# Optimization experiments

Hardware: AMD Instinct MI355X
Metric: run time of the kernel (lower is better)

Reference implementation:

```python
import jax, jax.numpy as jnp
import numpy as np

N_NODES = 50000
N_EDGES = 800000
IN_DIM = 128
HID = 64
NUM_GRAPHS = 64


def _gcn_conv(x, W, b, src, dst, num_nodes):
    """PyG GCNConv: out = D^-1/2 (A+I) D^-1/2 (x W) + b, messages scattered to dst."""
    h = x @ W  # [N, out]
    ones = jnp.ones((src.shape[0],), dtype=x.dtype)
    # degree at target nodes, self-loop adds 1
    deg = jax.ops.segment_sum(ones, dst, num_segments=num_nodes) + 1.0
    dinv = jax.lax.rsqrt(deg)  # [N]
    norm = dinv[src] * dinv[dst]  # [E]
    msgs = h[src] * norm[:, None]  # [E, out] gather-scale
    agg = jax.ops.segment_sum(msgs, dst, num_segments=num_nodes)  # scatter-add
    # self-loop contribution: norm_ii = dinv[i]^2
    agg = agg + h * (dinv * dinv)[:, None]
    return agg + b


def setup_inputs() -> dict:
    key = jax.random.key(0)
    k = jax.random.split(key, 10)
    x = jax.random.normal(k[0], (N_NODES, IN_DIM), dtype=jnp.float32)
    edge_index = jax.random.randint(k[1], (2, N_EDGES), 0, N_NODES, dtype=jnp.int32)
    batch = jnp.sort(jax.random.randint(k[2], (N_NODES,), 0, NUM_GRAPHS, dtype=jnp.int32))
    # Glorot-ish params
    W1 = jax.random.normal(k[3], (IN_DIM, HID), dtype=jnp.float32) / np.sqrt(IN_DIM)
    b1 = jnp.zeros((HID,), dtype=jnp.float32)
    W2 = jax.random.normal(k[4], (HID, HID), dtype=jnp.float32) / np.sqrt(HID)
    b2 = jnp.zeros((HID,), dtype=jnp.float32)
    Wlin = jax.random.normal(k[5], (HID, 1), dtype=jnp.float32) / np.sqrt(HID)
    blin = jnp.zeros((1,), dtype=jnp.float32)
    return {"x": x, "edge_index": edge_index, "batch": batch,
            "W1": W1, "b1": b1, "W2": W2, "b2": b2, "Wlin": Wlin, "blin": blin}


def reference(x, edge_index, batch, W1, b1, W2, b2, Wlin, blin):
    src, dst = edge_index[0], edge_index[1]
    h = _gcn_conv(x, W1, b1, src, dst, N_NODES)
    h = jax.nn.relu(h)  # dropout is identity in eval mode
    h = _gcn_conv(h, W2, b2, src, dst, N_NODES)
    h = jax.nn.relu(h)
    # global mean pool per graph
    sums = jax.ops.segment_sum(h, batch, num_segments=NUM_GRAPHS)  # [G, HID]
    cnts = jax.ops.segment_sum(jnp.ones((N_NODES,), h.dtype), batch, num_segments=NUM_GRAPHS)
    pooled = sums / jnp.maximum(cnts, 1.0)[:, None]
    return pooled @ Wlin + blin  # [G, 1]
```

## Files before the change

kernel.cpp:

```cpp
#include <hip/hip_runtime.h>
#include <hip/hip_fp16.h>

#define N_NODES 50000
#define N_EDGES 800000
#define IN_DIM 128
#define HID 64
#define NUM_GRAPHS 64
#define RED_BLOCKS 128
#define NB 196
#define NBLK 256

__device__ inline float4 load_h4(const __half* p) {
    const __half2* q = (const __half2*)p;
    float2 a = __half22float2(q[0]);
    float2 b = __half22float2(q[1]);
    return make_float4(a.x, a.y, b.x, b.y);
}
__device__ inline void store_h4(__half* p, float4 v) {
    __half2* q = (__half2*)p;
    q[0] = __floats2half2_rn(v.x, v.y);
    q[1] = __floats2half2_rn(v.z, v.w);
}

__global__ __launch_bounds__(256) void hist_kernel(const int* __restrict__ dst, int* __restrict__ hist_g) {
    __shared__ int h[NB];
    int tid = threadIdx.x;
    for (int i = tid; i < NB; i += 256) h[i] = 0;
    __syncthreads();
    const int NI = N_EDGES / 4;
    for (int i = blockIdx.x * 256 + tid; i < NI; i += NBLK * 256) {
        int4 d = ((const int4*)dst)[i];
        atomicAdd(&h[d.x >> 8], 1);
        atomicAdd(&h[d.y >> 8], 1);
        atomicAdd(&h[d.z >> 8], 1);
        atomicAdd(&h[d.w >> 8], 1);
    }
    __syncthreads();
    for (int i = tid; i < NB; i += 256) hist_g[i * NBLK + blockIdx.x] = h[i];
}

__global__ __launch_bounds__(1024) void scan2_kernel(const int* __restrict__ in, int* __restrict__ pos,
                                                     int* __restrict__ offs) {
    __shared__ int wsum[16];
    __shared__ int tot_s;
    int tid = threadIdx.x;
    int lane = tid & 63, wid = tid >> 6;
    int carry = 0;
    const int L = NB * NBLK;
    for (int base = 0; base < L; base += 4096) {
        int idx = base + tid * 4;
        int v0 = 0, v1 = 0, v2 = 0, v3 = 0;
        if (idx < L) { int4 v = *(const int4*)&in[idx]; v0 = v.x; v1 = v.y; v2 = v.z; v3 = v.w; }
        int s0 = v0, s1 = s0 + v1, s2 = s1 + v2, s3 = s2 + v3;
        int inc = s3;
        #pragma unroll
        for (int d = 1; d < 64; d <<= 1) { int t = __shfl_up(inc, d, 64); if (lane >= d) inc += t; }
        if (lane == 63) wsum[wid] = inc;
        __syncthreads();
        if (tid < 16) {
            int wv = wsum[tid], winc = wv;
            #pragma unroll
            for (int d = 1; d < 16; d <<= 1) { int t = __shfl_up(winc, d, 16); if (tid >= d) winc += t; }
            wsum[tid] = winc - wv;
            if (tid == 15) tot_s = winc;
        }
        __syncthreads();
        int excl = carry + wsum[wid] + inc - s3;
        if (idx < L) { int4 o; o.x = excl; o.y = excl + s0; o.z = excl + s1; o.w = excl + s2; *(int4*)&pos[idx] = o; }
        carry += tot_s;
    }
    if (tid == 0) offs[N_NODES] = N_EDGES;
}

__global__ __launch_bounds__(256) void bin_kernel(const int* __restrict__ src, const int* __restrict__ dst,
                                                  const int* __restrict__ pos, int* __restrict__ binned) {
    __shared__ int cur[NB];
    int tid = threadIdx.x;
    for (int i = tid; i < NB; i += 256) cur[i] = pos[i * NBLK + blockIdx.x];
    __syncthreads();
    const int NI = N_EDGES / 4;
    for (int i = blockIdx.x * 256 + tid; i < NI; i += NBLK * 256) {
        int4 s = ((const int4*)src)[i];
        int4 d = ((const int4*)dst)[i];
        int p0 = atomicAdd(&cur[d.x >> 8], 1); binned[p0] = (s.x & 0xFFFF) | ((d.x & 255) << 16);
        int p1 = atomicAdd(&cur[d.y >> 8], 1); binned[p1] = (s.y & 0xFFFF) | ((d.y & 255) << 16);
        int p2 = atomicAdd(&cur[d.z >> 8], 1); binned[p2] = (s.z & 0xFFFF) | ((d.z & 255) << 16);
        int p3 = atomicAdd(&cur[d.w >> 8], 1); binned[p3] = (s.w & 0xFFFF) | ((d.w & 255) << 16);
    }
}

__global__ __launch_bounds__(256) void build_kernel(const int* __restrict__ binned, const int* __restrict__ pos,
                                                    int* __restrict__ offs, float* __restrict__ dinv,
                                                    int* __restrict__ csr_src) {
    __shared__ int cnt[256];
    __shared__ int excl[256];
    __shared__ int rnk[256];
    __shared__ int wtot[4];
    int b = blockIdx.x, tid = threadIdx.x;
    int base = pos[b * NBLK];
    int end  = (b == NB - 1) ? N_EDGES : pos[(b + 1) * NBLK];
    cnt[tid] = 0; rnk[tid] = 0;
    __syncthreads();
    for (int j = base + tid; j < end; j += 256) atomicAdd(&cnt[(binned[j] >> 16) & 255], 1);
    __syncthreads();
    int v = cnt[tid];
    int lane = tid & 63, wid = tid >> 6;
    int inc = v;
    #pragma unroll
    for (int d = 1; d < 64; d <<= 1) { int t = __shfl_up(inc, d, 64); if (lane >= d) inc += t; }
    if (lane == 63) wtot[wid] = inc;
    __syncthreads();
    if (tid == 0) {
        int a = 0;
        for (int w = 0; w < 4; w++) { int t = wtot[w]; wtot[w] = a; a += t; }
    }
    __syncthreads();
    excl[tid] = wtot[wid] + inc - v;
    int node = b * 256 + tid;
    if (node < N_NODES) {
        offs[node] = base + excl[tid];
        dinv[node] = rsqrtf((float)v + 1.0f);
    }
    __syncthreads();
    for (int j = base + tid; j < end; j += 256) {
        int e = binned[j];
        int l = (e >> 16) & 255;
        int r = atomicAdd(&rnk[l], 1);
        csr_src[base + excl[l] + r] = e & 0xFFFF;
    }
}

template <int K, typename TIN>
__global__ __launch_bounds__(256) void gemm_kernel(const TIN* __restrict__ A, const float* __restrict__ W,
                                                   const float* __restrict__ dinv,
                                                   __half* __restrict__ out, int nRows) {
    constexpr int KB = 64;
    constexpr int KBP = KB + 4;
    __shared__ float xs[64 * KBP];
    __shared__ float ws[KB * 68];
    int tid = threadIdx.x;
    int node0 = blockIdx.x * 64;
    int c0 = (tid & 15) * 4, n0 = (tid >> 4) * 4;
    float acc[4][4] = {};
    for (int kb = 0; kb < K; kb += KB) {
        for (int i = tid; i < KB * 16; i += 256) {
            int k = i >> 4, c4 = (i & 15) * 4;
            *(float4*)&ws[k * 68 + c4] = *(const float4*)&W[(size_t)(kb + k) * 64 + c4];
        }
        for (int i = tid; i < 64 * (KB / 4); i += 256) {
            int n = i / (KB / 4), k4 = (i % (KB / 4)) * 4;
            int gn = node0 + n;
            float4 v;
            if (gn < nRows) {
                if constexpr (sizeof(TIN) == 4) v = *(const float4*)&A[(size_t)gn * K + kb + k4];
                else                            v = load_h4((const __half*)&A[(size_t)gn * K + kb + k4]);
            } else v = make_float4(0.f, 0.f, 0.f, 0.f);
            *(float4*)&xs[n * KBP + k4] = v;
        }
        __syncthreads();
        for (int k = 0; k < KB; k += 4) {
            float4 x0 = *(const float4*)&xs[(n0 + 0) * KBP + k];
            float4 x1 = *(const float4*)&xs[(n0 + 1) * KBP + k];
            float4 x2 = *(const float4*)&xs[(n0 + 2) * KBP + k];
            float4 x3 = *(const float4*)&xs[(n0 + 3) * KBP + k];
            #define KSTEP(KK, F) { \
                float4 wr = *(const float4*)&ws[(k + KK) * 68 + c0]; \
                acc[0][0] += x0.F * wr.x; acc[0][1] += x0.F * wr.y; acc[0][2] += x0.F * wr.z; acc[0][3] += x0.F * wr.w; \
                acc[1][0] += x1.F * wr.x; acc[1][1] += x1.F * wr.y; acc[1][2] += x1.F * wr.z; acc[1][3] += x1.F * wr.w; \
                acc[2][0] += x2.F * wr.x; acc[2][1] += x2.F * wr.y; acc[2][2] += x2.F * wr.z; acc[2][3] += x2.F * wr.w; \
                acc[3][0] += x3.F * wr.x; acc[3][1] += x3.F * wr.y; acc[3][2] += x3.F * wr.z; acc[3][3] += x3.F * wr.w; }
            KSTEP(0, x)
            KSTEP(1, y)
            KSTEP(2, z)
            KSTEP(3, w)
            #undef KSTEP
        }
        __syncthreads();
    }
    #pragma unroll
    for (int i = 0; i < 4; i++) {
        int gn = node0 + n0 + i;
        if (gn < nRows) {
            float sc = dinv[gn];
            store_h4(&out[(size_t)gn * 64 + c0],
                     make_float4(acc[i][0] * sc, acc[i][1] * sc, acc[i][2] * sc, acc[i][3] * sc));
        }
    }
}

__global__ __launch_bounds__(256) void agg_kernel(const __half* __restrict__ hd, const int* __restrict__ offs,
                                                  const int* __restrict__ csr_src,
                                                  const float* __restrict__ dinv, const float* __restrict__ bias,
                                                  __half* __restrict__ out) {
    int lane = threadIdx.x & 63;
    int node = blockIdx.x * 4 + (threadIdx.x >> 6);
    if (node >= N_NODES) return;
    int q = lane >> 4;
    int cc = (lane & 15) * 4;
    float4 acc = make_float4(0.f, 0.f, 0.f, 0.f);
    int beg = offs[node], end = offs[node + 1];
    #pragma unroll 2
    for (int j = beg + q; j < end; j += 4) {
        int s = csr_src[j];
        float4 hv = load_h4(&hd[(size_t)s * 64 + cc]);
        acc.x += hv.x; acc.y += hv.y; acc.z += hv.z; acc.w += hv.w;
    }
    #pragma unroll
    for (int m = 16; m <= 32; m <<= 1) {
        acc.x += __shfl_xor(acc.x, m, 64);
        acc.y += __shfl_xor(acc.y, m, 64);
        acc.z += __shfl_xor(acc.z, m, 64);
        acc.w += __shfl_xor(acc.w, m, 64);
    }
    if (q == 0) {
        float di = dinv[node];
        float4 hn = load_h4(&hd[(size_t)node * 64 + cc]);
        const float4 bv = *(const float4*)&bias[cc];
        float4 r;
        r.x = fmaxf(fmaf(di, acc.x + hn.x, bv.x), 0.0f);
        r.y = fmaxf(fmaf(di, acc.y + hn.y, bv.y), 0.0f);
        r.z = fmaxf(fmaf(di, acc.z + hn.z, bv.z), 0.0f);
        r.w = fmaxf(fmaf(di, acc.w + hn.w, bv.w), 0.0f);
        store_h4(&out[(size_t)node * 64 + cc], r);
    }
}

__global__ __launch_bounds__(256) void agg2dot_kernel(const __half* __restrict__ hd, const int* __restrict__ offs,
                                                      const int* __restrict__ csr_src,
                                                      const float* __restrict__ dinv, const float* __restrict__ bias,
                                                      const float* __restrict__ Wlin,
                                                      float* __restrict__ ndot) {
    int lane = threadIdx.x & 63;
    int node = blockIdx.x * 4 + (threadIdx.x >> 6);
    if (node >= N_NODES) return;
    int q = lane >> 4;
    int cc = (lane & 15) * 4;
    float4 acc = make_float4(0.f, 0.f, 0.f, 0.f);
    int beg = offs[node], end = offs[node + 1];
    #pragma unroll 2
    for (int j = beg + q; j < end; j += 4) {
        int s = csr_src[j];
        float4 hv = load_h4(&hd[(size_t)s * 64 + cc]);
        acc.x += hv.x; acc.y += hv.y; acc.z += hv.z; acc.w += hv.w;
    }
    #pragma unroll
    for (int m = 16; m <= 32; m <<= 1) {
        acc.x += __shfl_xor(acc.x, m, 64);
        acc.y += __shfl_xor(acc.y, m, 64);
        acc.z += __shfl_xor(acc.z, m, 64);
        acc.w += __shfl_xor(acc.w, m, 64);
    }
    if (q == 0) {
        float di = dinv[node];
        float4 hn = load_h4(&hd[(size_t)node * 64 + cc]);
        const float4 bv = *(const float4*)&bias[cc];
        const float4 wl = *(const float4*)&Wlin[cc];
        float rx = fmaxf(fmaf(di, acc.x + hn.x, bv.x), 0.0f);
        float ry = fmaxf(fmaf(di, acc.y + hn.y, bv.y), 0.0f);
        float rz = fmaxf(fmaf(di, acc.z + hn.z, bv.z), 0.0f);
        float rw = fmaxf(fmaf(di, acc.w + hn.w, bv.w), 0.0f);
        float d = rx * wl.x + ry * wl.y + rz * wl.z + rw * wl.w;
        #pragma unroll
        for (int m = 1; m < 16; m <<= 1) d += __shfl_xor(d, m, 64);
        if ((lane & 15) == 0) ndot[node] = d;
    }
}

__global__ __launch_bounds__(256) void reduce_kernel(const float* __restrict__ ndot, const int* __restrict__ batch,
                                                     float* __restrict__ gpart) {
    __shared__ float lsum[NUM_GRAPHS];
    __shared__ float lcnt[NUM_GRAPHS];
    int tid = threadIdx.x;
    if (tid < NUM_GRAPHS) { lsum[tid] = 0.0f; lcnt[tid] = 0.0f; }
    __syncthreads();
    for (int i = blockIdx.x * 256 + tid; i < N_NODES; i += RED_BLOCKS * 256) {
        atomicAdd(&lsum[batch[i]], ndot[i]);
        atomicAdd(&lcnt[batch[i]], 1.0f);
    }
    __syncthreads();
    if (tid < NUM_GRAPHS) {
        gpart[(size_t)blockIdx.x * (2 * NUM_GRAPHS) + tid] = lsum[tid];
        gpart[(size_t)blockIdx.x * (2 * NUM_GRAPHS) + NUM_GRAPHS + tid] = lcnt[tid];
    }
}

__global__ __launch_bounds__(1024) void final_kernel(const float* __restrict__ gpart, const float* __restrict__ blin,
                                                     float* __restrict__ out) {
    __shared__ float rs[1024];
    __shared__ float rc[1024];
    int tid = threadIdx.x;
    int g = tid & 63;
    int c = tid >> 6;
    float s = 0.0f, cn = 0.0f;
    for (int b = c; b < RED_BLOCKS; b += 16) {
        s  += gpart[(size_t)b * (2 * NUM_GRAPHS) + g];
        cn += gpart[(size_t)b * (2 * NUM_GRAPHS) + NUM_GRAPHS + g];
    }
    rs[tid] = s; rc[tid] = cn;
    __syncthreads();
    if (c == 0) {
        float ts = 0.0f, tc = 0.0f;
        #pragma unroll
        for (int k = 0; k < 16; k++) { ts += rs[k * 64 + g]; tc += rc[k * 64 + g]; }
        out[g] = ts / fmaxf(tc, 1.0f) + blin[0];
    }
}

extern "C" void kernel_launch(void* const* d_in, const int* in_sizes, int n_in,
                              void* d_out, int out_size, void* d_ws, size_t ws_size,
                              hipStream_t stream) {
    const float* x    = (const float*)d_in[0];
    const int*   ei   = (const int*)d_in[1];
    const int*   batch= (const int*)d_in[2];
    const float* W1   = (const float*)d_in[3];
    const float* b1   = (const float*)d_in[4];
    const float* W2   = (const float*)d_in[5];
    const float* b2   = (const float*)d_in[6];
    const float* Wlin = (const float*)d_in[7];
    const float* blin = (const float*)d_in[8];
    float* out = (float*)d_out;
    const int* srcA = ei;
    const int* dstA = ei + N_EDGES;

    char* p = (char*)d_ws;
    auto alloc = [&](size_t n) { char* r = p; p += (n + 255) & ~(size_t)255; return r; };
    int*    hist_g  = (int*)alloc((size_t)NB * NBLK * 4);
    int*    pos     = (int*)alloc((size_t)NB * NBLK * 4);
    int*    offs    = (int*)alloc((size_t)(N_NODES + 1) * 4);
    int*    binned  = (int*)alloc((size_t)N_EDGES * 4);
    int*    csr_src = (int*)alloc((size_t)N_EDGES * 4);
    float*  dinv    = (float*)alloc((size_t)N_NODES * 4);
    float*  ndot    = (float*)alloc((size_t)N_NODES * 4);
    float*  gpart   = (float*)alloc((size_t)RED_BLOCKS * 2 * NUM_GRAPHS * 4);
    __half* bufA    = (__half*)alloc((size_t)N_NODES * 64 * 2);
    __half* bufB    = (__half*)alloc((size_t)N_NODES * 64 * 2);

    hist_kernel<<<NBLK, 256, 0, stream>>>(dstA, hist_g);
    scan2_kernel<<<1, 1024, 0, stream>>>(hist_g, pos, offs);
    bin_kernel<<<NBLK, 256, 0, stream>>>(srcA, dstA, pos, binned);
    build_kernel<<<NB, 256, 0, stream>>>(binned, pos, offs, dinv, csr_src);

    gemm_kernel<IN_DIM, float><<<(N_NODES + 63) / 64, 256, 0, stream>>>(x, W1, dinv, bufA, N_NODES);
    agg_kernel<<<(N_NODES + 3) / 4, 256, 0, stream>>>(bufA, offs, csr_src, dinv, b1, bufB);
    gemm_kernel<HID, __half><<<(N_NODES + 63) / 64, 256, 0, stream>>>(bufB, W2, dinv, bufA, N_NODES);
    agg2dot_kernel<<<(N_NODES + 3) / 4, 256, 0, stream>>>(bufA, offs, csr_src, dinv, b2, Wlin, ndot);

    reduce_kernel<<<RED_BLOCKS, 256, 0, stream>>>(ndot, batch, gpart);
    final_kernel<<<1, 1024, 0, stream>>>(gpart, blin, out);
}
```

Before: 210.4 us.

## Replace two-stage atomic pooling with per-graph binary-search segmented reduction

Measured after the change: 209.4 us. About the same (-0.5%).

```diff
diff --git a/kernel.cpp b/kernel.cpp
--- a/kernel.cpp
+++ b/kernel.cpp
@@ -6,7 +6,6 @@
 #define IN_DIM 128
 #define HID 64
 #define NUM_GRAPHS 64
-#define RED_BLOCKS 128
 #define NB 196
 #define NBLK 256
 
@@ -266,43 +265,26 @@
     }
 }
 
-__global__ __launch_bounds__(256) void reduce_kernel(const float* __restrict__ ndot, const int* __restrict__ batch,
-                                                     float* __restrict__ gpart) {
-    __shared__ float lsum[NUM_GRAPHS];
-    __shared__ float lcnt[NUM_GRAPHS];
-    int tid = threadIdx.x;
-    if (tid < NUM_GRAPHS) { lsum[tid] = 0.0f; lcnt[tid] = 0.0f; }
-    __syncthreads();
-    for (int i = blockIdx.x * 256 + tid; i < N_NODES; i += RED_BLOCKS * 256) {
-        atomicAdd(&lsum[batch[i]], ndot[i]);
-        atomicAdd(&lcnt[batch[i]], 1.0f);
-    }
-    __syncthreads();
-    if (tid < NUM_GRAPHS) {
-        gpart[(size_t)blockIdx.x * (2 * NUM_GRAPHS) + tid] = lsum[tid];
-        gpart[(size_t)blockIdx.x * (2 * NUM_GRAPHS) + NUM_GRAPHS + tid] = lcnt[tid];
-    }
-}
-
-__global__ __launch_bounds__(1024) void final_kernel(const float* __restrict__ gpart, const float* __restrict__ blin,
-                                                     float* __restrict__ out) {
-    __shared__ float rs[1024];
-    __shared__ float rc[1024];
-    int tid = threadIdx.x;
-    int g = tid & 63;
-    int c = tid >> 6;
-    float s = 0.0f, cn = 0.0f;
-    for (int b = c; b < RED_BLOCKS; b += 16) {
-        s  += gpart[(size_t)b * (2 * NUM_GRAPHS) + g];
-        cn += gpart[(size_t)b * (2 * NUM_GRAPHS) + NUM_GRAPHS + g];
-    }
-    rs[tid] = s; rc[tid] = cn;
-    __syncthreads();
-    if (c == 0) {
-        float ts = 0.0f, tc = 0.0f;
-        #pragma unroll
-        for (int k = 0; k < 16; k++) { ts += rs[k * 64 + g]; tc += rc[k * 64 + g]; }
-        out[g] = ts / fmaxf(tc, 1.0f) + blin[0];
+__global__ __launch_bounds__(256) void graphred_kernel(const float* __restrict__ ndot, const int* __restrict__ batch,
+                                                       const float* __restrict__ blin, float* __restrict__ out) {
+    __shared__ float wpart[4];
+    int g = blockIdx.x;
+    int tid = threadIdx.x;
+    int lo = 0, hi = N_NODES;
+    while (lo < hi) { int m = (lo + hi) >> 1; if (batch[m] < g) lo = m + 1; else hi = m; }
+    int lo2 = lo, hi2 = N_NODES;
+    while (lo2 < hi2) { int m = (lo2 + hi2) >> 1; if (batch[m] < g + 1) lo2 = m + 1; else hi2 = m; }
+    float s = 0.0f;
+    for (int i = lo + tid; i < lo2; i += 256) s += ndot[i];
+    int lane = tid & 63, wid = tid >> 6;
+    #pragma unroll
+    for (int m = 32; m > 0; m >>= 1) s += __shfl_down(s, m, 64);
+    if (lane == 0) wpart[wid] = s;
+    __syncthreads();
+    if (tid == 0) {
+        float t = wpart[0] + wpart[1] + wpart[2] + wpart[3];
+        float cnt = (float)(lo2 - lo);
+        out[g] = t / fmaxf(cnt, 1.0f) + blin[0];
     }
 }
 
@@ -331,7 +313,6 @@
     int*    csr_src = (int*)alloc((size_t)N_EDGES * 4);
     float*  dinv    = (float*)alloc((size_t)N_NODES * 4);
     float*  ndot    = (float*)alloc((size_t)N_NODES * 4);
-    float*  gpart   = (float*)alloc((size_t)RED_BLOCKS * 2 * NUM_GRAPHS * 4);
     __half* bufA    = (__half*)alloc((size_t)N_NODES * 64 * 2);
     __half* bufB    = (__half*)alloc((size_t)N_NODES * 64 * 2);
 
@@ -345,6 +326,5 @@
     gemm_kernel<HID, __half><<<(N_NODES + 63) / 64, 256, 0, stream>>>(bufB, W2, dinv, bufA, N_NODES);
     agg2dot_kernel<<<(N_NODES + 3) / 4, 256, 0, stream>>>(bufA, offs, csr_src, dinv, b2, Wlin, ndot);
 
-    reduce_kernel<<<RED_BLOCKS, 256, 0, stream>>>(ndot, batch, gpart);
-    final_kernel<<<1, 1024, 0, stream>>>(gpart, blin, out);
-}
+    graphred_kernel<<<NUM_GRAPHS, 256, 0, stream>>>(ndot, batch, blin, out);
+}
```
